# Kernel optimization log

Hardware: AMD Instinct MI355X
Metric: run time of the kernel (lower is better)

## Reference

```python
import jax, jax.numpy as jnp
import numpy as np

B, N, C = 64, 256, 512
SHIFTS = (-1, 0, 1)
# torch.chunk(N, 3): ceil(256/3)=86 -> sizes [86, 86, 84]
CHUNK_SIZES = (86, 86, 84)
EPS = 1e-5


def _shift_pad(a, s):
    # shift along last axis (C) with zero padding, matching shift_with_padding
    if s == 0:
        return a
    if s > 0:
        return jnp.pad(a[..., :-s], ((0, 0), (0, 0), (s, 0)))
    s = -s
    return jnp.pad(a[..., s:], ((0, 0), (0, 0), (0, s)))


def setup_inputs() -> dict:
    key = jax.random.key(0)
    ks = jax.random.split(key, 16)
    w = lambda k, shape: (jax.random.normal(k, shape, jnp.float32) * 0.02)
    inp = {
        "x": jax.random.normal(ks[0], (B, N, C), jnp.float32),
        "ln_g": jnp.ones((C,), jnp.float32),
        "ln_b": jnp.zeros((C,), jnp.float32),
        "Ws": w(ks[1], (C, C)),
        "bs": jnp.zeros((C,), jnp.float32),
        "Wc": w(ks[2], (N, N, 3)),     # Conv1d weight [out=N, in=N, k=3]
        "bc": jnp.zeros((N,), jnp.float32),
        "We1": w(ks[3], (N, N // 8)),
        "be1": jnp.zeros((N // 8,), jnp.float32),
        "We2": w(ks[4], (N // 8, N)),
        "be2": jnp.zeros((N,), jnp.float32),
        "Wf1": w(ks[5], (C, 2 * C)),
        "bf1": jnp.zeros((2 * C,), jnp.float32),
        "Wf2": w(ks[6], (2 * C, C)),
        "bf2": jnp.zeros((C,), jnp.float32),
    }
    return inp


def reference(x, ln_g, ln_b, Ws, bs, Wc, bc, We1, be1, We2, be2, Wf1, bf1, Wf2, bf2):
    res = x
    # channel_mixer_S: LayerNorm over C, then Linear C->C + relu (dropout=0)
    mu = jnp.mean(x, axis=-1, keepdims=True)
    var = jnp.mean((x - mu) ** 2, axis=-1, keepdims=True)
    h = (x - mu) * jax.lax.rsqrt(var + EPS) * ln_g + ln_b
    h = jax.nn.relu(h @ Ws + bs)                      # [B, N, C]
    # channel_shift: chunk along N, shift each chunk along C with zero pad
    offs = np.cumsum((0,) + CHUNK_SIZES)
    chunks = [h[:, offs[i]:offs[i + 1], :] for i in range(3)]
    x_shift = jnp.concatenate([_shift_pad(c, s) for c, s in zip(chunks, SHIFTS)], axis=1)
    # channel_projection: Conv1d over C with N channels, k=3, pad=1
    x_shift = jax.lax.conv_general_dilated(
        x_shift, Wc, window_strides=(1,), padding=[(1, 1)],
        dimension_numbers=("NCH", "OIH", "NCH")) + bc[None, :, None]
    # SE gating
    se = jnp.mean(x_shift, axis=-1)                   # [B, N]
    ex = jax.nn.sigmoid(jax.nn.relu(se @ We1 + be1) @ We2 + be2)  # [B, N]
    z = x_shift * ex[:, :, None]
    # channel_mixer_F: C -> 2C (relu) -> C, residual
    z = jax.nn.relu(z @ Wf1 + bf1) @ Wf2 + bf2 + res
    return z
```

## Files before the change

kernel.cpp:

```cpp
#include <hip/hip_runtime.h>
#include <hip/hip_bf16.h>
#include <math.h>

#define BB 64
#define NN 256
#define CCH 512

typedef unsigned short u16;
typedef __attribute__((ext_vector_type(8))) short s16x8;
typedef __attribute__((ext_vector_type(4))) float f32x4;

#define AS1 __attribute__((address_space(1)))
#define AS3 __attribute__((address_space(3)))

static __device__ __forceinline__ u16 f2b(float f) {
    __hip_bfloat16 h = __float2bfloat16(f);
    union { __hip_bfloat16 h; u16 u; } x; x.h = h; return x.u;
}
static __device__ __forceinline__ void gll16(const void* g, void* l) {
    __builtin_amdgcn_global_load_lds((const AS1 unsigned int*)g,
                                     (AS3 unsigned int*)l, 16, 0, 0);
}

#define VM8  asm volatile("s_waitcnt vmcnt(8)" ::: "memory")
#define VM6  asm volatile("s_waitcnt vmcnt(6)" ::: "memory")
#define VM4  asm volatile("s_waitcnt vmcnt(4)" ::: "memory")
#define VM3  asm volatile("s_waitcnt vmcnt(3)" ::: "memory")
#define VM0  asm volatile("s_waitcnt vmcnt(0)" ::: "memory")
#define MEMB asm volatile("" ::: "memory")

static __device__ __forceinline__ void wtc_body(const float* __restrict__ W,
    u16* __restrict__ Wt, int K, int N, int bx, int by, float* t )
{
    int n0 = bx * 32, k0 = by * 32;
    int tx = threadIdx.x & 31, ty = threadIdx.x >> 5;
    #pragma unroll
    for (int i = 0; i < 4; ++i)
        t[(ty + i * 8) * 33 + tx] = W[(size_t)(k0 + ty + i * 8) * N + n0 + tx];
    __syncthreads();
    #pragma unroll
    for (int i = 0; i < 4; ++i)
        Wt[(size_t)(n0 + ty + i * 8) * K + k0 + tx] = f2b(t[tx * 33 + ty + i * 8]);
}

__global__ __launch_bounds__(256) void prep_ln_kernel(
    const float* __restrict__ Ws,  u16* __restrict__ Wst,
    const float* __restrict__ Wf1, u16* __restrict__ Wf1t,
    const float* __restrict__ Wf2, u16* __restrict__ Wf2t,
    const float* __restrict__ Wc,  u16* __restrict__ Wc3,
    u16* __restrict__ Hts,
    const float* __restrict__ x, const float* __restrict__ g,
    const float* __restrict__ bta, u16* __restrict__ xnorm)
{
    __shared__ float t[32 * 33];
    int bid = blockIdx.x;
    if (bid < 256) {
        wtc_body(Ws, Wst, 512, 512, bid & 15, bid >> 4, t);
    } else if (bid < 768) {
        int idx = bid - 256;
        wtc_body(Wf1, Wf1t, 512, 1024, idx & 31, idx >> 5, t);
    } else if (bid < 1280) {
        int idx = bid - 768;
        wtc_body(Wf2, Wf2t, 1024, 512, idx & 15, idx >> 4, t);
    } else if (bid < 2048) {
        int idx = (bid - 1280) * 256 + threadIdx.x;
        int i = idx & 255;
        int o = (idx >> 8) & 255;
        int k = idx >> 16;
        Wc3[idx] = f2b(Wc[((size_t)o * NN + i) * 3 + k]);
    } else if (bid < 2304) {
        int idx = (bid - 2048) * 256 + threadIdx.x;
        int b   = idx >> 10;
        int rem = idx & 1023;
        int rr  = rem >> 8;
        int r   = (rr & 1) + (rr >> 1) * 512;
        Hts[((size_t)b * 514 + r) * 256 + (rem & 255)] = 0;
    } else {
        const int l = threadIdx.x & 63;
        const int r = (bid - 2304) * 4 + (threadIdx.x >> 6);
        const float4* xr = (const float4*)(x + (size_t)r * CCH);
        float4 v1 = xr[l];
        float4 v2 = xr[l + 64];
        float s  = v1.x + v1.y + v1.z + v1.w + v2.x + v2.y + v2.z + v2.w;
        float ss = v1.x*v1.x + v1.y*v1.y + v1.z*v1.z + v1.w*v1.w
                 + v2.x*v2.x + v2.y*v2.y + v2.z*v2.z + v2.w*v2.w;
        #pragma unroll
        for (int o = 32; o > 0; o >>= 1) {
            s  += __shfl_xor(s, o);
            ss += __shfl_xor(ss, o);
        }
        float mu  = s * (1.0f / CCH);
        float var = ss * (1.0f / CCH) - mu * mu;
        float rs  = rsqrtf(var + 1e-5f);
        float4 g1 = ((const float4*)g)[l],   g2 = ((const float4*)g)[l + 64];
        float4 b1 = ((const float4*)bta)[l], b2 = ((const float4*)bta)[l + 64];
        ushort4 o1, o2;
        o1.x = f2b((v1.x - mu) * rs * g1.x + b1.x);
        o1.y = f2b((v1.y - mu) * rs * g1.y + b1.y);
        o1.z = f2b((v1.z - mu) * rs * g1.z + b1.z);
        o1.w = f2b((v1.w - mu) * rs * g1.w + b1.w);
        o2.x = f2b((v2.x - mu) * rs * g2.x + b2.x);
        o2.y = f2b((v2.y - mu) * rs * g2.y + b2.y);
        o2.z = f2b((v2.z - mu) * rs * g2.z + b2.z);
        o2.w = f2b((v2.w - mu) * rs * g2.w + b2.w);
        ushort4* orow = (ushort4*)(xnorm + (size_t)r * CCH);
        orow[l]      = o1;
        orow[l + 64] = o2;
    }
}

template<int MODE, int BNT>
__global__ __launch_bounds__(512, 1) void gemm_pipe(
    const u16* __restrict__ A, const u16* __restrict__ Bt,
    const float* __restrict__ bias, const float* __restrict__ scale,
    const float* __restrict__ res, void* __restrict__ outv,
    u16* __restrict__ auxout, float* __restrict__ SEpart)
{
    constexpr int NK = (MODE == 2) ? 32 : (MODE == 3) ? 24 : 16;
    constexpr int SA = (MODE == 2) ? 1024 : 512;
    constexpr int SB = (MODE == 2) ? 1024 : 512;
    constexpr int NOUT = (MODE == 1) ? 1024 : 512;
    constexpr int NF = BNT / 64;
    constexpr int BSZ = BNT * 32;

    __shared__ u16 Asm[4 * 256 * 32];
    __shared__ u16 Bsm[4 * BSZ];

    const int tid = threadIdx.x;
    const int l   = tid & 63;
    const int w   = tid >> 6;
    const int nwg = gridDim.x;
    const int work = (blockIdx.x & 7) * (nwg >> 3) + (blockIdx.x >> 3);

    int row0, col0, bidx = 0;
    if (MODE == 0)      { row0 = (work >> 7) * 256; col0 = (work & 127) * 128; }
    else if (MODE == 1) { row0 = (work >> 2) * 256; col0 = (work & 3) * 256; }
    else if (MODE == 2) { row0 = (work >> 2) * 256; col0 = (work & 3) * 128; }
    else                { row0 = 0; bidx = work >> 2; col0 = (work & 3) * 128; }

    const u16* Aab  = A + (size_t)row0 * SA;
    const u16* Bab  = Bt + (size_t)col0 * SB;
    const u16* HtsB = Bt + (size_t)bidx * 514 * 256;

    const int wm = (w >> 2) * 128;
    const int wn = (w & 3) * (BNT / 4);
    const int fr = l & 15;
    const int q  = l >> 4;
    const int kofs = ((q ^ ((l >> 1) & 3)) * 8);

    const f32x4 zero = {0.0f, 0.0f, 0.0f, 0.0f};
    f32x4 acc[8][NF];
    #pragma unroll
    for (int m = 0; m < 8; ++m)
        #pragma unroll
        for (int n = 0; n < NF; ++n) acc[m][n] = zero;

    const int kc0 = ((tid & 3) ^ ((tid >> 3) & 3)) * 8;
    const int srow = tid >> 2;

    auto stage = [&](int u) {
        const int slot = u & 3;
        u16* ald = Asm + slot * 8192 + w * 512;
        u16* bld = Bsm + slot * BSZ + w * 512;
        if (MODE == 3) {
            const int kseg = u >> 3, kb = (u & 7) * 32 + kc0;
            gll16(A + kseg * 65536 + srow * 256 + kb, ald);
            gll16(A + kseg * 65536 + (srow + 128) * 256 + kb, ald + 4096);
            gll16(HtsB + (size_t)(col0 + srow + kseg) * 256 + kb, bld);
        } else {
            const int kb = u * 32 + kc0;
            gll16(Aab + (size_t)srow * SA + kb, ald);
            gll16(Aab + (size_t)(srow + 128) * SA + kb, ald + 4096);
            gll16(Bab + (size_t)srow * SB + kb, bld);
            if (BNT == 256)
                gll16(Bab + (size_t)(srow + 128) * SB + kb, bld + 4096);
        }
    };

    stage(0); stage(1); stage(2);

    for (int u = 0; u < NK; ++u) {
        if (BNT == 128) {
            if (u < NK - 2)       { VM6; }
            else if (u == NK - 2) { VM3; }
            else                  { VM0; }
        } else {
            if (u < NK - 2)       { VM8; }
            else if (u == NK - 2) { VM4; }
            else                  { VM0; }
        }
        __builtin_amdgcn_s_barrier();
        MEMB;
        const int slot = u & 3;
        s16x8 bfv[NF];
        #pragma unroll
        for (int n = 0; n < NF; ++n)
            bfv[n] = *(const s16x8*)&Bsm[slot * BSZ + (wn + n * 16 + fr) * 32 + kofs];
        s16x8 af[8];
        #pragma unroll
        for (int m = 0; m < 8; ++m)
            af[m] = *(const s16x8*)&Asm[slot * 8192 + (wm + m * 16 + fr) * 32 + kofs];
        if (u + 3 < NK) stage(u + 3);
        __builtin_amdgcn_s_setprio(1);
        #pragma unroll
        for (int m = 0; m < 8; ++m)
            #pragma unroll
            for (int n = 0; n < NF; ++n)
                acc[m][n] = __builtin_amdgcn_mfma_f32_16x16x32_bf16(af[m], bfv[n], acc[m][n], 0, 0, 0);
        __builtin_amdgcn_s_setprio(0);
        MEMB;
    }

    if (MODE == 0) {
        #pragma unroll
        for (int m = 0; m < 8; ++m) {
            #pragma unroll
            for (int j = 0; j < 4; ++j) {
                const int c = row0 + wm + m * 16 + (l >> 4) * 4 + j;
                const float bsv = bias[c];
                #pragma unroll
                for (int n = 0; n < NF; ++n) {
                    const int gcol = col0 + wn + n * 16 + fr;
                    const int b  = gcol >> 8;
                    const int ni = gcol & 255;
                    const int s  = (ni < 86) ? -1 : (ni < 172 ? 0 : 1);
                    auxout[((size_t)b * 514 + c + 1 + s) * 256 + ni] =
                        f2b(fmaxf(acc[m][n][j] + bsv, 0.0f));
                }
            }
        }
    } else if (MODE == 1) {
        #pragma unroll
        for (int m = 0; m < 8; ++m) {
            #pragma unroll
            for (int j = 0; j < 4; ++j) {
                const int row = row0 + wm + m * 16 + (l >> 4) * 4 + j;
                const float sc = scale[row];
                #pragma unroll
                for (int n = 0; n < NF; ++n) {
                    const int col = col0 + wn + n * 16 + fr;
                    ((u16*)outv)[(size_t)row * NOUT + col] =
                        f2b(fmaxf(acc[m][n][j] * sc + bias[col], 0.0f));
                }
            }
        }
    } else if (MODE == 2) {
        #pragma unroll
        for (int m = 0; m < 8; ++m) {
            #pragma unroll
            for (int j = 0; j < 4; ++j) {
                const int row = row0 + wm + m * 16 + (l >> 4) * 4 + j;
                #pragma unroll
                for (int n = 0; n < NF; ++n) {
                    const int col = col0 + wn + n * 16 + fr;
                    ((float*)outv)[(size_t)row * NOUT + col] =
                        acc[m][n][j] + bias[col] + res[(size_t)row * NOUT + col];
                }
            }
        }
    } else {
        const int ct = col0 >> 7;
        #pragma unroll
        for (int m = 0; m < 8; ++m) {
            #pragma unroll
            for (int j = 0; j < 4; ++j) {
                const int no = wm + m * 16 + (l >> 4) * 4 + j;
                const float bcv = bias[no];
                float p = 0.0f;
                #pragma unroll
                for (int n = 0; n < NF; ++n) {
                    const int c = col0 + wn + n * 16 + fr;
                    float v = acc[m][n][j];
                    auxout[((size_t)bidx * NN + no) * CCH + c] = f2b(v + bcv);
                    p += v;
                }
                p += __shfl_xor(p, 1);
                p += __shfl_xor(p, 2);
                p += __shfl_xor(p, 4);
                p += __shfl_xor(p, 8);
                if (fr == 0)
                    SEpart[ct * 16384 + bidx * NN + no] = p;
            }
        }
    }
}

__global__ __launch_bounds__(256) void semlp_kernel(const float* __restrict__ sep,
    const float* __restrict__ bc,
    const float* __restrict__ We1, const float* __restrict__ be1,
    const float* __restrict__ We2, const float* __restrict__ be2,
    float* __restrict__ ex)
{
    __shared__ float sse[256];
    __shared__ float e1[32];
    int b = blockIdx.x, t = threadIdx.x;
    int o = b * 256 + t;
    sse[t] = (sep[o] + sep[16384 + o] + sep[32768 + o] + sep[49152 + o])
             * (1.0f / CCH) + bc[t];
    __syncthreads();
    if (t < 32) {
        float a = be1[t];
        #pragma unroll 8
        for (int i = 0; i < 256; ++i) a += sse[i] * We1[i * 32 + t];
        e1[t] = fmaxf(a, 0.0f);
    }
    __syncthreads();
    float a = be2[t];
    #pragma unroll
    for (int j = 0; j < 32; ++j) a += e1[j] * We2[j * 256 + t];
    ex[b * 256 + t] = 1.0f / (1.0f + expf(-a));
}

extern "C" void kernel_launch(void* const* d_in, const int* in_sizes, int n_in,
                              void* d_out, int out_size, void* d_ws, size_t ws_size,
                              hipStream_t stream) {
    const float* x    = (const float*)d_in[0];
    const float* ln_g = (const float*)d_in[1];
    const float* ln_b = (const float*)d_in[2];
    const float* Ws   = (const float*)d_in[3];
    const float* bs   = (const float*)d_in[4];
    const float* Wc   = (const float*)d_in[5];
    const float* bc   = (const float*)d_in[6];
    const float* We1  = (const float*)d_in[7];
    const float* be1  = (const float*)d_in[8];
    const float* We2  = (const float*)d_in[9];
    const float* be2  = (const float*)d_in[10];
    const float* Wf1  = (const float*)d_in[11];
    const float* bf1  = (const float*)d_in[12];
    const float* Wf2  = (const float*)d_in[13];
    const float* bf2  = (const float*)d_in[14];
    float* out = (float*)d_out;
    char* w8   = (char*)d_ws;

    u16* XN  = (u16*)(w8);
    u16* Y   = XN;
    u16* Hts = (u16*)(w8 + (16u << 20));
    u16* T   = (u16*)(w8 + (16u << 20));
    char* tail = w8 + 50397184;
    float* SEpart = (float*)(tail);
    float* EX     = (float*)(tail + 262144);
    u16* Wst      = (u16*)(tail + 327680);
    u16* Wf1t     = (u16*)(tail + 851968);
    u16* Wf2t     = (u16*)(tail + 1900544);
    u16* Wc3      = (u16*)(tail + 2949120);

    prep_ln_kernel<<<6400, 256, 0, stream>>>(Ws, Wst, Wf1, Wf1t, Wf2, Wf2t,
                                             Wc, Wc3, Hts, x, ln_g, ln_b, XN);
    gemm_pipe<0, 128><<<256, 512, 0, stream>>>(Wst, XN, bs, nullptr, nullptr,
                                               nullptr, Hts, nullptr);
    gemm_pipe<3, 128><<<256, 512, 0, stream>>>(Wc3, Hts, bc, nullptr, nullptr,
                                               nullptr, Y, SEpart);
    semlp_kernel<<<BB, 256, 0, stream>>>(SEpart, bc, We1, be1, We2, be2, EX);
    gemm_pipe<1, 256><<<256, 512, 0, stream>>>(Y, Wf1t, bf1, EX, nullptr,
                                               T, nullptr, nullptr);
    gemm_pipe<2, 128><<<256, 512, 0, stream>>>(T, Wf2t, bf2, nullptr, x,
                                               out, nullptr, nullptr);
}
```

Measured before the change: 115.4 us.

## Fuse SE MLP into FFN1 GEMM prologue and deepen BNT=128 pipeline

Removes the separate semlp kernel launch. Each FFN1 workgroup now recomputes the SE squeeze-excite MLP for its batch into shared memory while its first loads are in flight. The BNT=128 GEMMs switch from a 4-slot ring to a 6-slot ring that processes two k-steps per barrier, cutting barrier count and deepening prefetch. The cost is redundant SE MLP work in every FFN1 block and more LDS use.

```diff
diff --git a/kernel.cpp b/kernel.cpp
--- a/kernel.cpp
+++ b/kernel.cpp
@@ -25,8 +25,8 @@
 #define VM8  asm volatile("s_waitcnt vmcnt(8)" ::: "memory")
 #define VM6  asm volatile("s_waitcnt vmcnt(6)" ::: "memory")
 #define VM4  asm volatile("s_waitcnt vmcnt(4)" ::: "memory")
-#define VM3  asm volatile("s_waitcnt vmcnt(3)" ::: "memory")
 #define VM0  asm volatile("s_waitcnt vmcnt(0)" ::: "memory")
+#define LGKM0 asm volatile("s_waitcnt lgkmcnt(0)" ::: "memory")
 #define MEMB asm volatile("" ::: "memory")
 
 static __device__ __forceinline__ void wtc_body(const float* __restrict__ W,
@@ -112,9 +112,12 @@
 template<int MODE, int BNT>
 __global__ __launch_bounds__(512, 1) void gemm_pipe(
     const u16* __restrict__ A, const u16* __restrict__ Bt,
-    const float* __restrict__ bias, const float* __restrict__ scale,
-    const float* __restrict__ res, void* __restrict__ outv,
-    u16* __restrict__ auxout, float* __restrict__ SEpart)
+    const float* __restrict__ bias, const float* __restrict__ res,
+    void* __restrict__ outv, u16* __restrict__ auxout,
+    float* __restrict__ SEpart,
+    const float* __restrict__ seb, const float* __restrict__ We1,
+    const float* __restrict__ be1, const float* __restrict__ We2,
+    const float* __restrict__ be2)
 {
     constexpr int NK = (MODE == 2) ? 32 : (MODE == 3) ? 24 : 16;
     constexpr int SA = (MODE == 2) ? 1024 : 512;
@@ -122,9 +125,13 @@
     constexpr int NOUT = (MODE == 1) ? 1024 : 512;
     constexpr int NF = BNT / 64;
     constexpr int BSZ = BNT * 32;
-
-    __shared__ u16 Asm[4 * 256 * 32];
-    __shared__ u16 Bsm[4 * BSZ];
+    constexpr int NSLOT = (BNT == 128) ? 6 : 4;
+
+    __shared__ u16 Asm[NSLOT * 8192];
+    __shared__ u16 Bsm[NSLOT * BSZ];
+    __shared__ float sse[256];
+    __shared__ float e1f[32];
+    __shared__ float exs[256];
 
     const int tid = threadIdx.x;
     const int l   = tid & 63;
@@ -158,8 +165,7 @@
     const int kc0 = ((tid & 3) ^ ((tid >> 3) & 3)) * 8;
     const int srow = tid >> 2;
 
-    auto stage = [&](int u) {
-        const int slot = u & 3;
+    auto stage = [&](int u, int slot) {
         u16* ald = Asm + slot * 8192 + w * 512;
         u16* bld = Bsm + slot * BSZ + w * 512;
         if (MODE == 3) {
@@ -177,38 +183,105 @@
         }
     };
 
-    stage(0); stage(1); stage(2);
-
-    for (int u = 0; u < NK; ++u) {
-        if (BNT == 128) {
-            if (u < NK - 2)       { VM6; }
-            else if (u == NK - 2) { VM3; }
-            else                  { VM0; }
-        } else {
+    if (BNT == 128) {
+        stage(0, 0); stage(1, 1); stage(2, 2); stage(3, 3);
+        int sa = 0;
+        constexpr int NV = NK / 2;
+        for (int v = 0; v < NV; ++v) {
+            if (v + 1 < NV) { VM6; } else { VM0; }
+            __builtin_amdgcn_s_barrier();
+            MEMB;
+            const int sb = sa + 1;
+            s16x8 b0[2], af0[8];
+            #pragma unroll
+            for (int n = 0; n < 2; ++n)
+                b0[n] = *(const s16x8*)&Bsm[sa * BSZ + (wn + n * 16 + fr) * 32 + kofs];
+            #pragma unroll
+            for (int m = 0; m < 8; ++m)
+                af0[m] = *(const s16x8*)&Asm[sa * 8192 + (wm + m * 16 + fr) * 32 + kofs];
+            const int u2 = 2 * v + 4;
+            if (u2 < NK) {
+                int st = sa + 4; if (st >= 6) st -= 6;
+                stage(u2, st);
+                int st1 = st + 1; if (st1 >= 6) st1 -= 6;
+                stage(u2 + 1, st1);
+            }
+            __builtin_amdgcn_s_setprio(1);
+            #pragma unroll
+            for (int m = 0; m < 8; ++m)
+                #pragma unroll
+                for (int n = 0; n < 2; ++n)
+                    acc[m][n] = __builtin_amdgcn_mfma_f32_16x16x32_bf16(af0[m], b0[n], acc[m][n], 0, 0, 0);
+            __builtin_amdgcn_s_setprio(0);
+            s16x8 b1[2], af1[8];
+            #pragma unroll
+            for (int n = 0; n < 2; ++n)
+                b1[n] = *(const s16x8*)&Bsm[sb * BSZ + (wn + n * 16 + fr) * 32 + kofs];
+            #pragma unroll
+            for (int m = 0; m < 8; ++m)
+                af1[m] = *(const s16x8*)&Asm[sb * 8192 + (wm + m * 16 + fr) * 32 + kofs];
+            __builtin_amdgcn_s_setprio(1);
+            #pragma unroll
+            for (int m = 0; m < 8; ++m)
+                #pragma unroll
+                for (int n = 0; n < 2; ++n)
+                    acc[m][n] = __builtin_amdgcn_mfma_f32_16x16x32_bf16(af1[m], b1[n], acc[m][n], 0, 0, 0);
+            __builtin_amdgcn_s_setprio(0);
+            MEMB;
+            sa += 2; if (sa >= 6) sa = 0;
+        }
+    } else {
+        stage(0, 0); stage(1, 1); stage(2, 2);
+        if (MODE == 1) {
+            if (tid < 256) {
+                int o = row0 + tid;
+                sse[tid] = (SEpart[o] + SEpart[16384 + o] + SEpart[32768 + o]
+                            + SEpart[49152 + o]) * (1.0f / CCH) + seb[tid];
+            }
+            LGKM0;
+            __builtin_amdgcn_s_barrier();
+            if (tid < 32) {
+                float a = be1[tid];
+                #pragma unroll 8
+                for (int i = 0; i < 256; ++i) a += sse[i] * We1[i * 32 + tid];
+                e1f[tid] = fmaxf(a, 0.0f);
+            }
+            LGKM0;
+            __builtin_amdgcn_s_barrier();
+            if (tid < 256) {
+                float a = be2[tid];
+                #pragma unroll
+                for (int j = 0; j < 32; ++j) a += e1f[j] * We2[j * 256 + tid];
+                exs[tid] = 1.0f / (1.0f + expf(-a));
+            }
+            LGKM0;
+            __builtin_amdgcn_s_barrier();
+        }
+        for (int u = 0; u < NK; ++u) {
             if (u < NK - 2)       { VM8; }
             else if (u == NK - 2) { VM4; }
             else                  { VM0; }
-        }
-        __builtin_amdgcn_s_barrier();
-        MEMB;
-        const int slot = u & 3;
-        s16x8 bfv[NF];
-        #pragma unroll
-        for (int n = 0; n < NF; ++n)
-            bfv[n] = *(const s16x8*)&Bsm[slot * BSZ + (wn + n * 16 + fr) * 32 + kofs];
-        s16x8 af[8];
-        #pragma unroll
-        for (int m = 0; m < 8; ++m)
-            af[m] = *(const s16x8*)&Asm[slot * 8192 + (wm + m * 16 + fr) * 32 + kofs];
-        if (u + 3 < NK) stage(u + 3);
-        __builtin_amdgcn_s_setprio(1);
-        #pragma unroll
-        for (int m = 0; m < 8; ++m)
+            __builtin_amdgcn_s_barrier();
+            MEMB;
+            const int slot = u & 3;
+            s16x8 bfv[NF];
             #pragma unroll
             for (int n = 0; n < NF; ++n)
-                acc[m][n] = __builtin_amdgcn_mfma_f32_16x16x32_bf16(af[m], bfv[n], acc[m][n], 0, 0, 0);
-        __builtin_amdgcn_s_setprio(0);
-        MEMB;
+                bfv[n] = *(const s16x8*)&Bsm[slot * BSZ + (wn + n * 16 + fr) * 32 + kofs];
+            s16x8 af[8];
+            #pragma unroll
+            for (int m = 0; m < 8; ++m)
+                af[m] = *(const s16x8*)&Asm[slot * 8192 + (wm + m * 16 + fr) * 32 + kofs];
+            if (u + 3 < NK) stage(u + 3, (u + 3) & 3);
+            __builtin_amdgcn_s_setprio(1);
+            #pragma unroll
+            for (int m = 0; m < 8; ++m)
+                #pragma unroll
+                for (int n = 0; n < NF; ++n)
+                    acc[m][n] = __builtin_amdgcn_mfma_f32_16x16x32_bf16(af[m], bfv[n], acc[m][n], 0, 0, 0);
+            __builtin_amdgcn_s_setprio(0);
+            MEMB;
+        }
     }
 
     if (MODE == 0) {
@@ -234,8 +307,9 @@
         for (int m = 0; m < 8; ++m) {
             #pragma unroll
             for (int j = 0; j < 4; ++j) {
-                const int row = row0 + wm + m * 16 + (l >> 4) * 4 + j;
-                const float sc = scale[row];
+                const int rl  = wm + m * 16 + (l >> 4) * 4 + j;
+                const int row = row0 + rl;
+                const float sc = exs[rl];
                 #pragma unroll
                 for (int n = 0; n < NF; ++n) {
                     const int col = col0 + wn + n * 16 + fr;
@@ -283,32 +357,6 @@
             }
         }
     }
-}
-
-__global__ __launch_bounds__(256) void semlp_kernel(const float* __restrict__ sep,
-    const float* __restrict__ bc,
-    const float* __restrict__ We1, const float* __restrict__ be1,
-    const float* __restrict__ We2, const float* __restrict__ be2,
-    float* __restrict__ ex)
-{
-    __shared__ float sse[256];
-    __shared__ float e1[32];
-    int b = blockIdx.x, t = threadIdx.x;
-    int o = b * 256 + t;
-    sse[t] = (sep[o] + sep[16384 + o] + sep[32768 + o] + sep[49152 + o])
-             * (1.0f / CCH) + bc[t];
-    __syncthreads();
-    if (t < 32) {
-        float a = be1[t];
-        #pragma unroll 8
-        for (int i = 0; i < 256; ++i) a += sse[i] * We1[i * 32 + t];
-        e1[t] = fmaxf(a, 0.0f);
-    }
-    __syncthreads();
-    float a = be2[t];
-    #pragma unroll
-    for (int j = 0; j < 32; ++j) a += e1[j] * We2[j * 256 + t];
-    ex[b * 256 + t] = 1.0f / (1.0f + expf(-a));
 }
 
 extern "C" void kernel_launch(void* const* d_in, const int* in_sizes, int n_in,
@@ -338,21 +386,19 @@
     u16* T   = (u16*)(w8 + (16u << 20));
     char* tail = w8 + 50397184;
     float* SEpart = (float*)(tail);
-    float* EX     = (float*)(tail + 262144);
-    u16* Wst      = (u16*)(tail + 327680);
-    u16* Wf1t     = (u16*)(tail + 851968);
-    u16* Wf2t     = (u16*)(tail + 1900544);
-    u16* Wc3      = (u16*)(tail + 2949120);
+    u16* Wst      = (u16*)(tail + 262144);
+    u16* Wf1t     = (u16*)(tail + 786432);
+    u16* Wf2t     = (u16*)(tail + 1835008);
+    u16* Wc3      = (u16*)(tail + 2883584);
 
     prep_ln_kernel<<<6400, 256, 0, stream>>>(Ws, Wst, Wf1, Wf1t, Wf2, Wf2t,
                                              Wc, Wc3, Hts, x, ln_g, ln_b, XN);
-    gemm_pipe<0, 128><<<256, 512, 0, stream>>>(Wst, XN, bs, nullptr, nullptr,
-                                               nullptr, Hts, nullptr);
-    gemm_pipe<3, 128><<<256, 512, 0, stream>>>(Wc3, Hts, bc, nullptr, nullptr,
-                                               nullptr, Y, SEpart);
-    semlp_kernel<<<BB, 256, 0, stream>>>(SEpart, bc, We1, be1, We2, be2, EX);
-    gemm_pipe<1, 256><<<256, 512, 0, stream>>>(Y, Wf1t, bf1, EX, nullptr,
-                                               T, nullptr, nullptr);
-    gemm_pipe<2, 128><<<256, 512, 0, stream>>>(T, Wf2t, bf2, nullptr, x,
-                                               out, nullptr, nullptr);
-}
+    gemm_pipe<0, 128><<<256, 512, 0, stream>>>(Wst, XN, bs, nullptr,
+        nullptr, Hts, nullptr, nullptr, nullptr, nullptr, nullptr, nullptr);
+    gemm_pipe<3, 128><<<256, 512, 0, stream>>>(Wc3, Hts, bc, nullptr,
+        nullptr, Y, SEpart, nullptr, nullptr, nullptr, nullptr, nullptr);
+    gemm_pipe<1, 256><<<256, 512, 0, stream>>>(Y, Wf1t, bf1, nullptr,
+        T, nullptr, SEpart, bc, We1, be1, We2, be2);
+    gemm_pipe<2, 128><<<256, 512, 0, stream>>>(T, Wf2t, bf2, x,
+        out, nullptr, nullptr, nullptr, nullptr, nullptr, nullptr, nullptr);
+}
```

Result: no change. 116.5 us (+1.0%).

## Shrink GEMM tiles to 128x128 with 256-thread blocks and permuted-K vectorized epilogues

Applied to the files above, without the earlier changes.

All GEMM stages move from 256x128/256 tiles on 512-thread blocks (one per CU) to 128x128 tiles on 256-thread blocks, with two blocks allowed per CU and twice the grid size. The K dimension of the weight and intermediate layouts is permuted so each lane's four output columns become contiguous, which turns scattered bf16 stores into ushort4 stores. The SE partial sums are widened to 8 slices to match. The intent is better occupancy, better load balance across CUs and cheaper epilogue stores, at the cost of less data reuse per tile and more global loads.

```diff
diff --git a/kernel.cpp b/kernel.cpp
--- a/kernel.cpp
+++ b/kernel.cpp
@@ -21,16 +21,17 @@
     __builtin_amdgcn_global_load_lds((const AS1 unsigned int*)g,
                                      (AS3 unsigned int*)l, 16, 0, 0);
 }
+static __device__ __forceinline__ int shf(int ni) {
+    return (ni < 86) ? -1 : (ni < 172 ? 0 : 1);
+}
 
 #define VM8  asm volatile("s_waitcnt vmcnt(8)" ::: "memory")
-#define VM6  asm volatile("s_waitcnt vmcnt(6)" ::: "memory")
 #define VM4  asm volatile("s_waitcnt vmcnt(4)" ::: "memory")
-#define VM3  asm volatile("s_waitcnt vmcnt(3)" ::: "memory")
 #define VM0  asm volatile("s_waitcnt vmcnt(0)" ::: "memory")
 #define MEMB asm volatile("" ::: "memory")
 
 static __device__ __forceinline__ void wtc_body(const float* __restrict__ W,
-    u16* __restrict__ Wt, int K, int N, int bx, int by, float* t )
+    u16* __restrict__ Wt, int K, int N, int bx, int by, float* t, bool perm)
 {
     int n0 = bx * 32, k0 = by * 32;
     int tx = threadIdx.x & 31, ty = threadIdx.x >> 5;
@@ -38,9 +39,11 @@
     for (int i = 0; i < 4; ++i)
         t[(ty + i * 8) * 33 + tx] = W[(size_t)(k0 + ty + i * 8) * N + n0 + tx];
     __syncthreads();
+    int kl = k0 + tx;
+    int kp = perm ? ((kl & ~63) | ((kl & 15) << 2) | ((kl >> 4) & 3)) : kl;
     #pragma unroll
     for (int i = 0; i < 4; ++i)
-        Wt[(size_t)(n0 + ty + i * 8) * K + k0 + tx] = f2b(t[tx * 33 + ty + i * 8]);
+        Wt[(size_t)(n0 + ty + i * 8) * K + kp] = f2b(t[tx * 33 + ty + i * 8]);
 }
 
 __global__ __launch_bounds__(256) void prep_ln_kernel(
@@ -55,19 +58,20 @@
     __shared__ float t[32 * 33];
     int bid = blockIdx.x;
     if (bid < 256) {
-        wtc_body(Ws, Wst, 512, 512, bid & 15, bid >> 4, t);
+        wtc_body(Ws, Wst, 512, 512, bid & 15, bid >> 4, t, false);
     } else if (bid < 768) {
         int idx = bid - 256;
-        wtc_body(Wf1, Wf1t, 512, 1024, idx & 31, idx >> 5, t);
+        wtc_body(Wf1, Wf1t, 512, 1024, idx & 31, idx >> 5, t, true);
     } else if (bid < 1280) {
         int idx = bid - 768;
-        wtc_body(Wf2, Wf2t, 1024, 512, idx & 15, idx >> 4, t);
+        wtc_body(Wf2, Wf2t, 1024, 512, idx & 15, idx >> 4, t, true);
     } else if (bid < 2048) {
         int idx = (bid - 1280) * 256 + threadIdx.x;
-        int i = idx & 255;
+        int xloc = idx & 255;
         int o = (idx >> 8) & 255;
         int k = idx >> 16;
-        Wc3[idx] = f2b(Wc[((size_t)o * NN + i) * 3 + k]);
+        int il = (xloc & ~63) | ((xloc & 63) >> 2) | ((xloc & 3) << 4);
+        Wc3[idx] = f2b(Wc[((size_t)o * NN + il) * 3 + k]);
     } else if (bid < 2304) {
         int idx = (bid - 2048) * 256 + threadIdx.x;
         int b   = idx >> 10;
@@ -109,22 +113,19 @@
     }
 }
 
-template<int MODE, int BNT>
-__global__ __launch_bounds__(512, 1) void gemm_pipe(
+template<int MODE>
+__global__ __launch_bounds__(256, 2) void gemm_pipe(
     const u16* __restrict__ A, const u16* __restrict__ Bt,
-    const float* __restrict__ bias, const float* __restrict__ scale,
-    const float* __restrict__ res, void* __restrict__ outv,
-    u16* __restrict__ auxout, float* __restrict__ SEpart)
+    const float* __restrict__ bias, const float* __restrict__ res,
+    void* __restrict__ outv, u16* __restrict__ auxout,
+    float* __restrict__ SEpart, const float* __restrict__ EX)
 {
     constexpr int NK = (MODE == 2) ? 32 : (MODE == 3) ? 24 : 16;
     constexpr int SA = (MODE == 2) ? 1024 : 512;
     constexpr int SB = (MODE == 2) ? 1024 : 512;
-    constexpr int NOUT = (MODE == 1) ? 1024 : 512;
-    constexpr int NF = BNT / 64;
-    constexpr int BSZ = BNT * 32;
-
-    __shared__ u16 Asm[4 * 256 * 32];
-    __shared__ u16 Bsm[4 * BSZ];
+
+    __shared__ u16 Asm[4 * 4096];
+    __shared__ u16 Bsm[4 * 4096];
 
     const int tid = threadIdx.x;
     const int l   = tid & 63;
@@ -133,153 +134,163 @@
     const int work = (blockIdx.x & 7) * (nwg >> 3) + (blockIdx.x >> 3);
 
     int row0, col0, bidx = 0;
-    if (MODE == 0)      { row0 = (work >> 7) * 256; col0 = (work & 127) * 128; }
-    else if (MODE == 1) { row0 = (work >> 2) * 256; col0 = (work & 3) * 256; }
-    else if (MODE == 2) { row0 = (work >> 2) * 256; col0 = (work & 3) * 128; }
-    else                { row0 = 0; bidx = work >> 2; col0 = (work & 3) * 128; }
+    if (MODE == 0)      { row0 = (work >> 7) * 128; col0 = (work & 127) * 128; }
+    else if (MODE == 1) { row0 = (work >> 3) * 128; col0 = (work & 7) * 128; }
+    else if (MODE == 2) { row0 = (work >> 2) * 128; col0 = (work & 3) * 128; }
+    else                { bidx = work >> 3; row0 = ((work >> 2) & 1) * 128;
+                          col0 = (work & 3) * 128; }
 
     const u16* Aab  = A + (size_t)row0 * SA;
     const u16* Bab  = Bt + (size_t)col0 * SB;
     const u16* HtsB = Bt + (size_t)bidx * 514 * 256;
 
-    const int wm = (w >> 2) * 128;
-    const int wn = (w & 3) * (BNT / 4);
+    const int wm = (w >> 1) * 64;
+    const int wn = (w & 1) * 64;
     const int fr = l & 15;
     const int q  = l >> 4;
     const int kofs = ((q ^ ((l >> 1) & 3)) * 8);
 
     const f32x4 zero = {0.0f, 0.0f, 0.0f, 0.0f};
-    f32x4 acc[8][NF];
-    #pragma unroll
-    for (int m = 0; m < 8; ++m)
-        #pragma unroll
-        for (int n = 0; n < NF; ++n) acc[m][n] = zero;
+    f32x4 acc[4][4];
+    #pragma unroll
+    for (int m = 0; m < 4; ++m)
+        #pragma unroll
+        for (int n = 0; n < 4; ++n) acc[m][n] = zero;
 
     const int kc0 = ((tid & 3) ^ ((tid >> 3) & 3)) * 8;
     const int srow = tid >> 2;
 
-    auto stage = [&](int u) {
-        const int slot = u & 3;
-        u16* ald = Asm + slot * 8192 + w * 512;
-        u16* bld = Bsm + slot * BSZ + w * 512;
+    auto stage = [&](int u, int slot) {
+        u16* ald = Asm + slot * 4096 + w * 512;
+        u16* bld = Bsm + slot * 4096 + w * 512;
         if (MODE == 3) {
             const int kseg = u >> 3, kb = (u & 7) * 32 + kc0;
-            gll16(A + kseg * 65536 + srow * 256 + kb, ald);
-            gll16(A + kseg * 65536 + (srow + 128) * 256 + kb, ald + 4096);
+            gll16(A + kseg * 65536 + (row0 + srow) * 256 + kb, ald);
+            gll16(A + kseg * 65536 + (row0 + srow + 64) * 256 + kb, ald + 2048);
             gll16(HtsB + (size_t)(col0 + srow + kseg) * 256 + kb, bld);
+            gll16(HtsB + (size_t)(col0 + srow + 64 + kseg) * 256 + kb, bld + 2048);
         } else {
             const int kb = u * 32 + kc0;
             gll16(Aab + (size_t)srow * SA + kb, ald);
-            gll16(Aab + (size_t)(srow + 128) * SA + kb, ald + 4096);
+            gll16(Aab + (size_t)(srow + 64) * SA + kb, ald + 2048);
             gll16(Bab + (size_t)srow * SB + kb, bld);
-            if (BNT == 256)
-                gll16(Bab + (size_t)(srow + 128) * SB + kb, bld + 4096);
+            gll16(Bab + (size_t)(srow + 64) * SB + kb, bld + 2048);
         }
     };
 
-    stage(0); stage(1); stage(2);
-
+    stage(0, 0); stage(1, 1); stage(2, 2);
     for (int u = 0; u < NK; ++u) {
-        if (BNT == 128) {
-            if (u < NK - 2)       { VM6; }
-            else if (u == NK - 2) { VM3; }
-            else                  { VM0; }
-        } else {
-            if (u < NK - 2)       { VM8; }
-            else if (u == NK - 2) { VM4; }
-            else                  { VM0; }
-        }
+        if (u < NK - 2)       { VM8; }
+        else if (u == NK - 2) { VM4; }
+        else                  { VM0; }
         __builtin_amdgcn_s_barrier();
         MEMB;
         const int slot = u & 3;
-        s16x8 bfv[NF];
-        #pragma unroll
-        for (int n = 0; n < NF; ++n)
-            bfv[n] = *(const s16x8*)&Bsm[slot * BSZ + (wn + n * 16 + fr) * 32 + kofs];
-        s16x8 af[8];
-        #pragma unroll
-        for (int m = 0; m < 8; ++m)
-            af[m] = *(const s16x8*)&Asm[slot * 8192 + (wm + m * 16 + fr) * 32 + kofs];
-        if (u + 3 < NK) stage(u + 3);
+        s16x8 bf4[4], af[4];
+        #pragma unroll
+        for (int n = 0; n < 4; ++n)
+            bf4[n] = *(const s16x8*)&Bsm[slot * 4096 + (wn + n * 16 + fr) * 32 + kofs];
+        #pragma unroll
+        for (int m = 0; m < 4; ++m)
+            af[m] = *(const s16x8*)&Asm[slot * 4096 + (wm + m * 16 + fr) * 32 + kofs];
+        if (u + 3 < NK) stage(u + 3, (u + 3) & 3);
         __builtin_amdgcn_s_setprio(1);
         #pragma unroll
-        for (int m = 0; m < 8; ++m)
-            #pragma unroll
-            for (int n = 0; n < NF; ++n)
-                acc[m][n] = __builtin_amdgcn_mfma_f32_16x16x32_bf16(af[m], bfv[n], acc[m][n], 0, 0, 0);
+        for (int m = 0; m < 4; ++m)
+            #pragma unroll
+            for (int n = 0; n < 4; ++n)
+                acc[m][n] = __builtin_amdgcn_mfma_f32_16x16x32_bf16(af[m], bf4[n], acc[m][n], 0, 0, 0);
         __builtin_amdgcn_s_setprio(0);
         MEMB;
     }
 
     if (MODE == 0) {
-        #pragma unroll
-        for (int m = 0; m < 8; ++m) {
+        const int gb = col0 + wn;
+        const int b  = gb >> 8;
+        const int gl = gb & 255;
+        const int nib = gl + fr;
+        u16* HtsW = auxout + (size_t)b * 514 * 256;
+        const int px = gl + 4 * fr;
+        const int s0 = shf(nib), s3 = shf(nib + 48);
+        #pragma unroll
+        for (int m = 0; m < 4; ++m) {
             #pragma unroll
             for (int j = 0; j < 4; ++j) {
-                const int c = row0 + wm + m * 16 + (l >> 4) * 4 + j;
+                const int c = row0 + wm + m * 16 + q * 4 + j;
                 const float bsv = bias[c];
+                u16 vv[4];
                 #pragma unroll
-                for (int n = 0; n < NF; ++n) {
-                    const int gcol = col0 + wn + n * 16 + fr;
-                    const int b  = gcol >> 8;
-                    const int ni = gcol & 255;
-                    const int s  = (ni < 86) ? -1 : (ni < 172 ? 0 : 1);
-                    auxout[((size_t)b * 514 + c + 1 + s) * 256 + ni] =
-                        f2b(fmaxf(acc[m][n][j] + bsv, 0.0f));
+                for (int n = 0; n < 4; ++n)
+                    vv[n] = f2b(fmaxf(acc[m][n][j] + bsv, 0.0f));
+                if (s0 == s3) {
+                    ushort4 v4 = {vv[0], vv[1], vv[2], vv[3]};
+                    *(ushort4*)&HtsW[(size_t)(c + 1 + s0) * 256 + px] = v4;
+                } else {
+                    #pragma unroll
+                    for (int n = 0; n < 4; ++n)
+                        HtsW[(size_t)(c + 1 + shf(nib + n * 16)) * 256 + px + n] = vv[n];
                 }
             }
         }
     } else if (MODE == 1) {
-        #pragma unroll
-        for (int m = 0; m < 8; ++m) {
+        const int cgb = col0 + wn;
+        float bval[4];
+        #pragma unroll
+        for (int n = 0; n < 4; ++n) bval[n] = bias[cgb + n * 16 + fr];
+        #pragma unroll
+        for (int m = 0; m < 4; ++m) {
             #pragma unroll
             for (int j = 0; j < 4; ++j) {
-                const int row = row0 + wm + m * 16 + (l >> 4) * 4 + j;
-                const float sc = scale[row];
+                const int row = row0 + wm + m * 16 + q * 4 + j;
+                const float sc = EX[row];
+                u16 vv[4];
                 #pragma unroll
-                for (int n = 0; n < NF; ++n) {
+                for (int n = 0; n < 4; ++n)
+                    vv[n] = f2b(fmaxf(acc[m][n][j] * sc + bval[n], 0.0f));
+                ushort4 v4 = {vv[0], vv[1], vv[2], vv[3]};
+                *(ushort4*)&((u16*)outv)[(size_t)row * 1024 + cgb + 4 * fr] = v4;
+            }
+        }
+    } else if (MODE == 2) {
+        #pragma unroll
+        for (int m = 0; m < 4; ++m) {
+            #pragma unroll
+            for (int j = 0; j < 4; ++j) {
+                const int row = row0 + wm + m * 16 + q * 4 + j;
+                #pragma unroll
+                for (int n = 0; n < 4; ++n) {
                     const int col = col0 + wn + n * 16 + fr;
-                    ((u16*)outv)[(size_t)row * NOUT + col] =
-                        f2b(fmaxf(acc[m][n][j] * sc + bias[col], 0.0f));
+                    ((float*)outv)[(size_t)row * 512 + col] =
+                        acc[m][n][j] + bias[col] + res[(size_t)row * 512 + col];
                 }
             }
         }
-    } else if (MODE == 2) {
-        #pragma unroll
-        for (int m = 0; m < 8; ++m) {
+    } else {
+        const int cb = col0 + wn;
+        const int px = cb + 4 * fr;
+        const int sslot = cb >> 6;
+        #pragma unroll
+        for (int m = 0; m < 4; ++m) {
             #pragma unroll
             for (int j = 0; j < 4; ++j) {
-                const int row = row0 + wm + m * 16 + (l >> 4) * 4 + j;
-                #pragma unroll
-                for (int n = 0; n < NF; ++n) {
-                    const int col = col0 + wn + n * 16 + fr;
-                    ((float*)outv)[(size_t)row * NOUT + col] =
-                        acc[m][n][j] + bias[col] + res[(size_t)row * NOUT + col];
-                }
-            }
-        }
-    } else {
-        const int ct = col0 >> 7;
-        #pragma unroll
-        for (int m = 0; m < 8; ++m) {
-            #pragma unroll
-            for (int j = 0; j < 4; ++j) {
-                const int no = wm + m * 16 + (l >> 4) * 4 + j;
+                const int no = row0 + wm + m * 16 + q * 4 + j;
                 const float bcv = bias[no];
                 float p = 0.0f;
+                u16 vv[4];
                 #pragma unroll
-                for (int n = 0; n < NF; ++n) {
-                    const int c = col0 + wn + n * 16 + fr;
+                for (int n = 0; n < 4; ++n) {
                     float v = acc[m][n][j];
-                    auxout[((size_t)bidx * NN + no) * CCH + c] = f2b(v + bcv);
+                    vv[n] = f2b(v + bcv);
                     p += v;
                 }
+                ushort4 v4 = {vv[0], vv[1], vv[2], vv[3]};
+                *(ushort4*)&auxout[((size_t)bidx * NN + no) * CCH + px] = v4;
                 p += __shfl_xor(p, 1);
                 p += __shfl_xor(p, 2);
                 p += __shfl_xor(p, 4);
                 p += __shfl_xor(p, 8);
                 if (fr == 0)
-                    SEpart[ct * 16384 + bidx * NN + no] = p;
+                    SEpart[sslot * 16384 + bidx * NN + no] = p;
             }
         }
     }
@@ -295,8 +306,10 @@
     __shared__ float e1[32];
     int b = blockIdx.x, t = threadIdx.x;
     int o = b * 256 + t;
-    sse[t] = (sep[o] + sep[16384 + o] + sep[32768 + o] + sep[49152 + o])
-             * (1.0f / CCH) + bc[t];
+    float sum = 0.0f;
+    #pragma unroll
+    for (int i = 0; i < 8; ++i) sum += sep[i * 16384 + o];
+    sse[t] = sum * (1.0f / CCH) + bc[t];
     __syncthreads();
     if (t < 32) {
         float a = be1[t];
@@ -338,21 +351,21 @@
     u16* T   = (u16*)(w8 + (16u << 20));
     char* tail = w8 + 50397184;
     float* SEpart = (float*)(tail);
-    float* EX     = (float*)(tail + 262144);
-    u16* Wst      = (u16*)(tail + 327680);
-    u16* Wf1t     = (u16*)(tail + 851968);
-    u16* Wf2t     = (u16*)(tail + 1900544);
-    u16* Wc3      = (u16*)(tail + 2949120);
+    u16* Wst      = (u16*)(tail + 524288);
+    u16* Wf1t     = (u16*)(tail + 1048576);
+    u16* Wf2t     = (u16*)(tail + 2097152);
+    u16* Wc3      = (u16*)(tail + 3145728);
+    float* EX     = (float*)(tail + 3538944);
 
     prep_ln_kernel<<<6400, 256, 0, stream>>>(Ws, Wst, Wf1, Wf1t, Wf2, Wf2t,
                                              Wc, Wc3, Hts, x, ln_g, ln_b, XN);
-    gemm_pipe<0, 128><<<256, 512, 0, stream>>>(Wst, XN, bs, nullptr, nullptr,
-                                               nullptr, Hts, nullptr);
-    gemm_pipe<3, 128><<<256, 512, 0, stream>>>(Wc3, Hts, bc, nullptr, nullptr,
-                                               nullptr, Y, SEpart);
+    gemm_pipe<0><<<512, 256, 0, stream>>>(Wst, XN, bs, nullptr,
+        nullptr, Hts, nullptr, nullptr);
+    gemm_pipe<3><<<512, 256, 0, stream>>>(Wc3, Hts, bc, nullptr,
+        nullptr, Y, SEpart, nullptr);
     semlp_kernel<<<BB, 256, 0, stream>>>(SEpart, bc, We1, be1, We2, be2, EX);
-    gemm_pipe<1, 256><<<256, 512, 0, stream>>>(Y, Wf1t, bf1, EX, nullptr,
-                                               T, nullptr, nullptr);
-    gemm_pipe<2, 128><<<256, 512, 0, stream>>>(T, Wf2t, bf2, nullptr, x,
-                                               out, nullptr, nullptr);
-}
+    gemm_pipe<1><<<1024, 256, 0, stream>>>(Y, Wf1t, bf1, nullptr,
+        T, nullptr, nullptr, EX);
+    gemm_pipe<2><<<512, 256, 0, stream>>>(T, Wf2t, bf2, x,
+        out, nullptr, nullptr, nullptr);
+}
```

After: 117.5 us. No clear change (+1.9%).
